# Kernel tuning notes

Hardware: AMD Instinct MI355X
Metric: run time of the kernel (lower is better)

The kernel has to match this reference:

```python
import jax, jax.numpy as jnp
import numpy as np

H_HEADS = 16
STATE_N = 64

def setup_inputs() -> dict:
    key = jax.random.key(0)
    ks = jax.random.split(key, 9)
    B, T, D = 2, 1024, 1024
    H, ch, N = H_HEADS, D // H_HEADS, STATE_N
    inp = jax.random.normal(ks[0], (B, T, D), dtype=jnp.float32)
    # lin_logA params scaled so exp(cumsum(logA)) stays bounded (decaying state)
    W_logA = jax.random.normal(ks[1], (H, 1, ch), dtype=jnp.float32) * 0.01
    b_logA = jnp.full((H, 1), -0.05, dtype=jnp.float32)
    W_XBC = jax.random.normal(ks[3], (H, ch + 2 * N, ch), dtype=jnp.float32) * (1.0 / np.sqrt(ch))
    b_XBC = jax.random.normal(ks[4], (H, ch + 2 * N), dtype=jnp.float32) * 0.02
    W_gate = jax.random.normal(ks[5], (H, ch, ch), dtype=jnp.float32) * (1.0 / np.sqrt(ch))
    b_gate = jax.random.normal(ks[6], (H, ch), dtype=jnp.float32) * 0.02
    W_out = jax.random.normal(ks[7], (D, D), dtype=jnp.float32) * (1.0 / np.sqrt(D))
    b_out = jax.random.normal(ks[8], (D,), dtype=jnp.float32) * 0.02
    return {"inp": inp, "W_logA": W_logA, "b_logA": b_logA, "W_XBC": W_XBC,
            "b_XBC": b_XBC, "W_gate": W_gate, "b_gate": b_gate,
            "W_out": W_out, "b_out": b_out}

def _mamba2_forward(inp, W_logA, b_logA, W_XBC, b_XBC, W_gate, b_gate, W_out, b_out):
    B, T, D = inp.shape
    H, N = H_HEADS, STATE_N
    ch = D // H
    x = inp.reshape(B, T, H, ch)  # B,T,H,ch
    # MultiheadLinear: matmul((H,out,in), x[...,None]) + bias
    logA = jnp.einsum('hoc,bthc->btho', W_logA, x)[..., 0] + b_logA[:, 0]  # B,T,H
    XBC = jax.nn.silu(jnp.einsum('hoc,bthc->btho', W_XBC, x) + b_XBC)     # B,T,H,ch+2N
    X = XBC[..., :ch]                 # B,T,H,ch
    Bm = XBC[..., ch:ch + N]          # B,T,H,N
    Cm = XBC[..., ch + N:]            # B,T,H,N
    # quadratic SSM: A_ss[b,h,i,j] = exp(cum[i]-cum[j]) for j<=i else 0
    cum = jnp.cumsum(jnp.swapaxes(logA, 1, 2), axis=-1)  # B,H,T
    diff = cum[..., :, None] - cum[..., None, :]          # B,H,T,T
    causal = jnp.tril(jnp.ones((T, T), dtype=bool))
    A_ss = jnp.where(causal, jnp.exp(jnp.where(causal, diff, 0.0)), 0.0)  # B,H,T,T
    G = jnp.einsum('bihn,bjhn->bhij', Cm, Bm)             # B,H,T,T (C_i . B_j)
    Y = jnp.einsum('bhij,bjhc->bihc', A_ss * G, X)        # B,T,H,ch
    gate = jnp.einsum('hoc,bthc->btho', W_gate, x) + b_gate
    Yg = (gate * Y).reshape(B, T, D)
    return Yg @ W_out.T + b_out

def reference(inp, W_logA, b_logA, W_XBC, b_XBC, W_gate, b_gate, W_out, b_out):
    return _mamba2_forward(inp, W_logA, b_logA, W_XBC, b_XBC, W_gate, b_gate, W_out, b_out)
```

## Files before the change

kernel.cpp:

```cpp
#include <hip/hip_runtime.h>

typedef unsigned int   u32;
typedef unsigned short u16;
typedef __attribute__((ext_vector_type(8))) short bf16x8;
typedef __attribute__((ext_vector_type(4))) float f32x4;

__device__ __forceinline__ float bfs(u16 u) {
  union { u32 i; float f; } v; v.i = ((u32)u) << 16; return v.f;
}
__device__ __forceinline__ u16 f2bf(float f) {
  union { float f; u32 i; } v; v.f = f;
  u32 r = v.i + 0x7fffu + ((v.i >> 16) & 1u);
  return (u16)(r >> 16);
}
__device__ __forceinline__ ushort4 f2bf4(float4 v) {
  ushort4 p; p.x = f2bf(v.x); p.y = f2bf(v.y); p.z = f2bf(v.z); p.w = f2bf(v.w);
  return p;
}

__global__ __launch_bounds__(256) void k_proj(
    const float* __restrict__ inp,
    const float* __restrict__ W_XBC,  const float* __restrict__ b_XBC,
    const float* __restrict__ W_gate, const float* __restrict__ b_gate,
    const float* __restrict__ W_logA, const float* __restrict__ b_logA,
    u16* __restrict__ XsT, u16* __restrict__ Bms, u16* __restrict__ Cms,
    u16* __restrict__ gates, float* __restrict__ logAs)
{
  int tt = blockIdx.x, h = blockIdx.y;
  int tid = threadIdx.x;
  int w = tid >> 6, l = tid & 63, q = l >> 4, lr = l & 15;
  int m0 = tt * 64;
  int b = m0 >> 10, tl0 = m0 & 1023;
  int bh = b * 16 + h;

  __shared__ u16 Xt[64][72];
  __shared__ u16 Wt[256][72];
  __shared__ float wl[64];

  if (tid < 64) wl[tid] = W_logA[h * 64 + tid];
#pragma unroll
  for (int i = 0; i < 4; ++i) {
    int f = tid + 256 * i; int r = f >> 4, cq = f & 15;
    float4 xv = *(const float4*)(inp + (size_t)(m0 + r) * 1024 + h * 64 + 4 * cq);
    *(ushort4*)&Xt[r][4 * cq] = f2bf4(xv);
  }
#pragma unroll
  for (int i = 0; i < 16; ++i) {
    int f = tid + 256 * i; int r = f >> 4, cq = f & 15;
    const float* wsrc = (r < 192) ? (W_XBC + ((size_t)h * 192 + r) * 64)
                                  : (W_gate + ((size_t)h * 64 + (r - 192)) * 64);
    *(ushort4*)&Wt[r][4 * cq] = f2bf4(*(const float4*)(wsrc + 4 * cq));
  }
  __syncthreads();

  bf16x8 af[4][2];
#pragma unroll
  for (int rt = 0; rt < 4; ++rt) {
    af[rt][0] = *(const bf16x8*)&Xt[16 * rt + lr][q * 8];
    af[rt][1] = *(const bf16x8*)&Xt[16 * rt + lr][32 + q * 8];
  }

  f32x4 acc[4][4];
#pragma unroll
  for (int rt = 0; rt < 4; ++rt)
#pragma unroll
    for (int ct = 0; ct < 4; ++ct) acc[rt][ct] = (f32x4){0.f, 0.f, 0.f, 0.f};

#pragma unroll
  for (int ct = 0; ct < 4; ++ct) {
    bf16x8 b0 = *(const bf16x8*)&Wt[64 * w + 16 * ct + lr][q * 8];
    bf16x8 b1 = *(const bf16x8*)&Wt[64 * w + 16 * ct + lr][32 + q * 8];
#pragma unroll
    for (int rt = 0; rt < 4; ++rt) {
      acc[rt][ct] = __builtin_amdgcn_mfma_f32_16x16x32_bf16(af[rt][0], b0, acc[rt][ct], 0, 0, 0);
      acc[rt][ct] = __builtin_amdgcn_mfma_f32_16x16x32_bf16(af[rt][1], b1, acc[rt][ct], 0, 0, 0);
    }
  }

  if (tid < 64) {
    float a = b_logA[h];
#pragma unroll 16
    for (int k = 0; k < 64; ++k) a += bfs(Xt[tid][k]) * wl[k];
    logAs[(size_t)bh * 1024 + tl0 + tid] = a;
  }

  if (w == 0) {
#pragma unroll
    for (int ct = 0; ct < 4; ++ct) {
      int n = 16 * ct + lr;
      float bias = b_XBC[h * 192 + n];
#pragma unroll
      for (int rt = 0; rt < 4; ++rt) {
        float4 v;
#pragma unroll
        for (int r = 0; r < 4; ++r) {
          float s = acc[rt][ct][r] + bias;
          (&v.x)[r] = s / (1.f + __expf(-s));
        }
        *(ushort4*)(XsT + ((size_t)bh * 64 + n) * 1024 + tl0 + 16 * rt + q * 4) = f2bf4(v);
      }
    }
  } else if (w < 3) {
    u16* dst = (w == 1) ? Bms : Cms;
    int nbase = h * 192 + 64 * w;
#pragma unroll
    for (int ct = 0; ct < 4; ++ct) {
      int n = 16 * ct + lr;
      float bias = b_XBC[nbase + n];
#pragma unroll
      for (int rt = 0; rt < 4; ++rt)
#pragma unroll
        for (int r = 0; r < 4; ++r) {
          int tloc = tl0 + 16 * rt + q * 4 + r;
          float s = acc[rt][ct][r] + bias;
          s = s / (1.f + __expf(-s));
          dst[((size_t)bh * 1024 + tloc) * 64 + n] = f2bf(s);
        }
    }
  } else {
#pragma unroll
    for (int ct = 0; ct < 4; ++ct) {
      int n = 16 * ct + lr;
      float bias = b_gate[h * 64 + n];
#pragma unroll
      for (int rt = 0; rt < 4; ++rt)
#pragma unroll
        for (int r = 0; r < 4; ++r) {
          int tg = m0 + 16 * rt + q * 4 + r;
          gates[((size_t)tg * 16 + h) * 64 + n] = f2bf(acc[rt][ct][r] + bias);
        }
    }
  }
}

__global__ __launch_bounds__(1024) void k_scan(float* __restrict__ logAs)
{
  int bh = blockIdx.x;
  int t = threadIdx.x;
  __shared__ float buf0[1024], buf1[1024];
  buf0[t] = logAs[(size_t)bh * 1024 + t];
  __syncthreads();
  float* src = buf0; float* dstp = buf1;
  for (int off = 1; off < 1024; off <<= 1) {
    float v = src[t];
    if (t >= off) v += src[t - off];
    dstp[t] = v;
    __syncthreads();
    float* tmp = src; src = dstp; dstp = tmp;
  }
  logAs[(size_t)bh * 1024 + t] = src[t];
}

__global__ __launch_bounds__(256) void k_wconv(
    const float* __restrict__ Wout, u16* __restrict__ WoutB)
{
  int i = blockIdx.x * 256 + threadIdx.x;
  float4 v = ((const float4*)Wout)[i];
  ((ushort4*)WoutB)[i] = f2bf4(v);
}

__global__ __launch_bounds__(256) void k_ssm(
    const u16* __restrict__ XsT, const u16* __restrict__ Bms, const u16* __restrict__ Cms,
    const float* __restrict__ cum, const u16* __restrict__ gates, u16* __restrict__ Yg)
{
  int g = blockIdx.x >> 5;
  int bh = blockIdx.x & 31;
  int it = (g & 1) ? (g >> 1) : (15 - (g >> 1));
  int b = bh >> 4, h = bh & 15;

  const u16* Xb = XsT + (size_t)bh * 64 * 1024;
  const u16* Bb = Bms + (size_t)bh * 1024 * 64;
  const u16* Cb = Cms + (size_t)bh * 1024 * 64;
  const float* cumb = cum + bh * 1024;

  int tid = threadIdx.x;
  int w = tid >> 6, l = tid & 63, q = l >> 4, lr = l & 15;

  __shared__ u16 Cts[64][72];
  __shared__ u16 Bts[64][72];
  __shared__ u16 Xts[64][72];
  __shared__ u16 Sts[64][72];
  __shared__ float cumi[64], cumj[64];

  int i0 = it * 64;
#pragma unroll
  for (int i = 0; i < 4; ++i) {
    int f = tid + 256 * i; int r = f >> 4, cq = f & 15;
    *(ushort4*)&Cts[r][4 * cq] = *(const ushort4*)(Cb + (size_t)(i0 + r) * 64 + 4 * cq);
  }
  if (tid < 64) cumi[tid] = cumb[i0 + tid];
  __syncthreads();

  bf16x8 ca0 = *(const bf16x8*)&Cts[16 * w + lr][q * 8];
  bf16x8 ca1 = *(const bf16x8*)&Cts[16 * w + lr][32 + q * 8];

  f32x4 acc[4];
#pragma unroll
  for (int ct = 0; ct < 4; ++ct) acc[ct] = (f32x4){0.f, 0.f, 0.f, 0.f};

  for (int jt = 0; jt <= it; ++jt) {
    int j0 = jt * 64;
    __syncthreads();
#pragma unroll
    for (int i = 0; i < 4; ++i) {
      int f = tid + 256 * i; int r = f >> 4, cq = f & 15;
      *(ushort4*)&Bts[r][4 * cq] = *(const ushort4*)(Bb + (size_t)(j0 + r) * 64 + 4 * cq);
      *(ushort4*)&Xts[r][4 * cq] = *(const ushort4*)(Xb + (size_t)r * 1024 + j0 + 4 * cq);
    }
    if (tid < 64) cumj[tid] = cumb[j0 + tid];
    __syncthreads();

    bool diag = (jt == it);
#pragma unroll
    for (int ct = 0; ct < 4; ++ct) {
      f32x4 s = (f32x4){0.f, 0.f, 0.f, 0.f};
      bf16x8 b0 = *(const bf16x8*)&Bts[16 * ct + lr][q * 8];
      bf16x8 b1 = *(const bf16x8*)&Bts[16 * ct + lr][32 + q * 8];
      s = __builtin_amdgcn_mfma_f32_16x16x32_bf16(ca0, b0, s, 0, 0, 0);
      s = __builtin_amdgcn_mfma_f32_16x16x32_bf16(ca1, b1, s, 0, 0, 0);
      int jl = 16 * ct + lr;
      float cj = cumj[jl];
#pragma unroll
      for (int r = 0; r < 4; ++r) {
        int il = 16 * w + q * 4 + r;
        float v;
        if (diag && jl > il) v = 0.f;
        else v = s[r] * __expf(fminf(cumi[il] - cj, 30.f));
        Sts[il][jl] = f2bf(v);
      }
    }

    bf16x8 sa0 = *(const bf16x8*)&Sts[16 * w + lr][q * 8];
    bf16x8 sa1 = *(const bf16x8*)&Sts[16 * w + lr][32 + q * 8];
#pragma unroll
    for (int ct = 0; ct < 4; ++ct) {
      bf16x8 x0 = *(const bf16x8*)&Xts[16 * ct + lr][q * 8];
      bf16x8 x1 = *(const bf16x8*)&Xts[16 * ct + lr][32 + q * 8];
      acc[ct] = __builtin_amdgcn_mfma_f32_16x16x32_bf16(sa0, x0, acc[ct], 0, 0, 0);
      acc[ct] = __builtin_amdgcn_mfma_f32_16x16x32_bf16(sa1, x1, acc[ct], 0, 0, 0);
    }
  }

#pragma unroll
  for (int ct = 0; ct < 4; ++ct) {
    int c = 16 * ct + lr;
#pragma unroll
    for (int r = 0; r < 4; ++r) {
      int tg = i0 + 16 * w + q * 4 + r;
      size_t row = (size_t)(b * 1024 + tg);
      float gt = bfs(gates[(row * 16 + h) * 64 + c]);
      Yg[row * 1024 + h * 64 + c] = f2bf(acc[ct][r] * gt);
    }
  }
}

__global__ __launch_bounds__(256) void k_out(
    const u16* __restrict__ Yg, const u16* __restrict__ WoutB,
    const float* __restrict__ bout, float* __restrict__ out)
{
  int bm = blockIdx.x, bn = blockIdx.y;
  int tid = threadIdx.x;
  int w = tid >> 6, l = tid & 63, q = l >> 4, lr = l & 15;
  int m0 = bm * 128, d0 = bn * 64;

  __shared__ u16 Yt[128][72];
  __shared__ u16 Wt[64][72];

  f32x4 acc[2][4];
#pragma unroll
  for (int rt = 0; rt < 2; ++rt)
#pragma unroll
    for (int ct = 0; ct < 4; ++ct) acc[rt][ct] = (f32x4){0.f, 0.f, 0.f, 0.f};

  for (int kt = 0; kt < 16; ++kt) {
    int k0 = kt * 64;
#pragma unroll
    for (int i = 0; i < 8; ++i) {
      int f = tid + 256 * i; int r = f >> 4, cq = f & 15;
      *(ushort4*)&Yt[r][4 * cq] = *(const ushort4*)(Yg + (size_t)(m0 + r) * 1024 + k0 + 4 * cq);
    }
#pragma unroll
    for (int i = 0; i < 4; ++i) {
      int f = tid + 256 * i; int r = f >> 4, cq = f & 15;
      *(ushort4*)&Wt[r][4 * cq] = *(const ushort4*)(WoutB + (size_t)(d0 + r) * 1024 + k0 + 4 * cq);
    }
    __syncthreads();

    bf16x8 a00 = *(const bf16x8*)&Yt[32 * w + lr][q * 8];
    bf16x8 a01 = *(const bf16x8*)&Yt[32 * w + lr][32 + q * 8];
    bf16x8 a10 = *(const bf16x8*)&Yt[32 * w + 16 + lr][q * 8];
    bf16x8 a11 = *(const bf16x8*)&Yt[32 * w + 16 + lr][32 + q * 8];
#pragma unroll
    for (int ct = 0; ct < 4; ++ct) {
      bf16x8 b0 = *(const bf16x8*)&Wt[16 * ct + lr][q * 8];
      bf16x8 b1 = *(const bf16x8*)&Wt[16 * ct + lr][32 + q * 8];
      acc[0][ct] = __builtin_amdgcn_mfma_f32_16x16x32_bf16(a00, b0, acc[0][ct], 0, 0, 0);
      acc[0][ct] = __builtin_amdgcn_mfma_f32_16x16x32_bf16(a01, b1, acc[0][ct], 0, 0, 0);
      acc[1][ct] = __builtin_amdgcn_mfma_f32_16x16x32_bf16(a10, b0, acc[1][ct], 0, 0, 0);
      acc[1][ct] = __builtin_amdgcn_mfma_f32_16x16x32_bf16(a11, b1, acc[1][ct], 0, 0, 0);
    }
    __syncthreads();
  }

#pragma unroll
  for (int rt = 0; rt < 2; ++rt)
#pragma unroll
    for (int ct = 0; ct < 4; ++ct) {
      int d = d0 + 16 * ct + lr;
      float bo = bout[d];
#pragma unroll
      for (int r = 0; r < 4; ++r) {
        int m = m0 + 32 * w + 16 * rt + q * 4 + r;
        out[(size_t)m * 1024 + d] = acc[rt][ct][r] + bo;
      }
    }
}

extern "C" void kernel_launch(void* const* d_in, const int* in_sizes, int n_in,
                              void* d_out, int out_size, void* d_ws, size_t ws_size,
                              hipStream_t stream)
{
  const float* inp   = (const float*)d_in[0];
  const float* WlogA = (const float*)d_in[1];
  const float* blogA = (const float*)d_in[2];
  const float* WXBC  = (const float*)d_in[3];
  const float* bXBC  = (const float*)d_in[4];
  const float* Wgate = (const float*)d_in[5];
  const float* bgate = (const float*)d_in[6];
  const float* Wout  = (const float*)d_in[7];
  const float* bout  = (const float*)d_in[8];
  float* out = (float*)d_out;

  const size_t SZ = (size_t)2 * 16 * 1024 * 64;
  float* logAs = (float*)d_ws;
  u16* base16  = (u16*)(logAs + 32768);
  u16* XsT   = base16;
  u16* Bms   = XsT + SZ;
  u16* Cms   = Bms + SZ;
  u16* gates = Cms + SZ;
  u16* Yg    = gates + SZ;
  u16* WoutB = Yg + SZ;

  k_proj<<<dim3(32, 16), 256, 0, stream>>>(inp, WXBC, bXBC, Wgate, bgate,
                                           WlogA, blogA, XsT, Bms, Cms, gates, logAs);
  k_scan<<<32, 1024, 0, stream>>>(logAs);
  k_wconv<<<1024, 256, 0, stream>>>(Wout, WoutB);
  k_ssm<<<dim3(512), 256, 0, stream>>>(XsT, Bms, Cms, logAs, gates, Yg);
  k_out<<<dim3(16, 16), 256, 0, stream>>>(Yg, WoutB, bout, out);
}
```

Before: 137.4 us.

## Factor decay exp, prefetch tiles in SSM and output GEMM, shuffle-based scan

The scan kernel becomes a warp-shuffle prefix sum and also writes exp(cum) and exp(-cum) per timestep. The SSM kernel then multiplies these factors instead of computing an exponential per score element. Both the SSM and output-projection kernels now prefetch the next K/B/X tiles into registers while computing the current one. The output GEMM uses 512 threads per block, with each wave handling 16 rows. The factorised exponent drops the old clamp, so large cumulative decay could overflow or lose precision.

```diff
diff --git a/kernel.cpp b/kernel.cpp
--- a/kernel.cpp
+++ b/kernel.cpp
@@ -133,22 +133,35 @@
   }
 }
 
-__global__ __launch_bounds__(1024) void k_scan(float* __restrict__ logAs)
+__global__ __launch_bounds__(1024) void k_scan(
+    const float* __restrict__ logAs, float* __restrict__ rowexp,
+    float* __restrict__ colexp)
 {
   int bh = blockIdx.x;
   int t = threadIdx.x;
-  __shared__ float buf0[1024], buf1[1024];
-  buf0[t] = logAs[(size_t)bh * 1024 + t];
+  int wv = t >> 6, ln = t & 63;
+  __shared__ float wsum[16];
+  float v = logAs[(size_t)bh * 1024 + t];
+#pragma unroll
+  for (int off = 1; off < 64; off <<= 1) {
+    float n = __shfl_up(v, off, 64);
+    if (ln >= off) v += n;
+  }
+  if (ln == 63) wsum[wv] = v;
   __syncthreads();
-  float* src = buf0; float* dstp = buf1;
-  for (int off = 1; off < 1024; off <<= 1) {
-    float v = src[t];
-    if (t >= off) v += src[t - off];
-    dstp[t] = v;
-    __syncthreads();
-    float* tmp = src; src = dstp; dstp = tmp;
-  }
-  logAs[(size_t)bh * 1024 + t] = src[t];
+  if (wv == 0) {
+    float s = (ln < 16) ? wsum[ln] : 0.f;
+#pragma unroll
+    for (int off = 1; off < 16; off <<= 1) {
+      float n = __shfl_up(s, off, 64);
+      if (ln >= off) s += n;
+    }
+    if (ln < 16) wsum[ln] = s;
+  }
+  __syncthreads();
+  if (wv > 0) v += wsum[wv - 1];
+  rowexp[(size_t)bh * 1024 + t] = __expf(v);
+  colexp[(size_t)bh * 1024 + t] = __expf(-v);
 }
 
 __global__ __launch_bounds__(256) void k_wconv(
@@ -161,7 +174,8 @@
 
 __global__ __launch_bounds__(256) void k_ssm(
     const u16* __restrict__ XsT, const u16* __restrict__ Bms, const u16* __restrict__ Cms,
-    const float* __restrict__ cum, const u16* __restrict__ gates, u16* __restrict__ Yg)
+    const float* __restrict__ rowexp, const float* __restrict__ colexp,
+    const u16* __restrict__ gates, u16* __restrict__ Yg)
 {
   int g = blockIdx.x >> 5;
   int bh = blockIdx.x & 31;
@@ -171,7 +185,6 @@
   const u16* Xb = XsT + (size_t)bh * 64 * 1024;
   const u16* Bb = Bms + (size_t)bh * 1024 * 64;
   const u16* Cb = Cms + (size_t)bh * 1024 * 64;
-  const float* cumb = cum + bh * 1024;
 
   int tid = threadIdx.x;
   int w = tid >> 6, l = tid & 63, q = l >> 4, lr = l & 15;
@@ -180,7 +193,7 @@
   __shared__ u16 Bts[64][72];
   __shared__ u16 Xts[64][72];
   __shared__ u16 Sts[64][72];
-  __shared__ float cumi[64], cumj[64];
+  __shared__ float ref_[64], cef[64];
 
   int i0 = it * 64;
 #pragma unroll
@@ -188,7 +201,7 @@
     int f = tid + 256 * i; int r = f >> 4, cq = f & 15;
     *(ushort4*)&Cts[r][4 * cq] = *(const ushort4*)(Cb + (size_t)(i0 + r) * 64 + 4 * cq);
   }
-  if (tid < 64) cumi[tid] = cumb[i0 + tid];
+  if (tid < 64) ref_[tid] = rowexp[(size_t)bh * 1024 + i0 + tid];
   __syncthreads();
 
   bf16x8 ca0 = *(const bf16x8*)&Cts[16 * w + lr][q * 8];
@@ -198,17 +211,36 @@
 #pragma unroll
   for (int ct = 0; ct < 4; ++ct) acc[ct] = (f32x4){0.f, 0.f, 0.f, 0.f};
 
+  ushort4 pb[4], px[4]; float pce = 0.f;
+#pragma unroll
+  for (int i = 0; i < 4; ++i) {
+    int f = tid + 256 * i; int r = f >> 4, cq = f & 15;
+    pb[i] = *(const ushort4*)(Bb + (size_t)r * 64 + 4 * cq);
+    px[i] = *(const ushort4*)(Xb + (size_t)r * 1024 + 4 * cq);
+  }
+  if (tid < 64) pce = colexp[(size_t)bh * 1024 + tid];
+
   for (int jt = 0; jt <= it; ++jt) {
-    int j0 = jt * 64;
     __syncthreads();
 #pragma unroll
     for (int i = 0; i < 4; ++i) {
       int f = tid + 256 * i; int r = f >> 4, cq = f & 15;
-      *(ushort4*)&Bts[r][4 * cq] = *(const ushort4*)(Bb + (size_t)(j0 + r) * 64 + 4 * cq);
-      *(ushort4*)&Xts[r][4 * cq] = *(const ushort4*)(Xb + (size_t)r * 1024 + j0 + 4 * cq);
-    }
-    if (tid < 64) cumj[tid] = cumb[j0 + tid];
+      *(ushort4*)&Bts[r][4 * cq] = pb[i];
+      *(ushort4*)&Xts[r][4 * cq] = px[i];
+    }
+    if (tid < 64) cef[tid] = pce;
     __syncthreads();
+
+    if (jt < it) {
+      int j1 = (jt + 1) * 64;
+#pragma unroll
+      for (int i = 0; i < 4; ++i) {
+        int f = tid + 256 * i; int r = f >> 4, cq = f & 15;
+        pb[i] = *(const ushort4*)(Bb + (size_t)(j1 + r) * 64 + 4 * cq);
+        px[i] = *(const ushort4*)(Xb + (size_t)r * 1024 + j1 + 4 * cq);
+      }
+      if (tid < 64) pce = colexp[(size_t)bh * 1024 + j1 + tid];
+    }
 
     bool diag = (jt == it);
 #pragma unroll
@@ -219,13 +251,11 @@
       s = __builtin_amdgcn_mfma_f32_16x16x32_bf16(ca0, b0, s, 0, 0, 0);
       s = __builtin_amdgcn_mfma_f32_16x16x32_bf16(ca1, b1, s, 0, 0, 0);
       int jl = 16 * ct + lr;
-      float cj = cumj[jl];
+      float cj = cef[jl];
 #pragma unroll
       for (int r = 0; r < 4; ++r) {
         int il = 16 * w + q * 4 + r;
-        float v;
-        if (diag && jl > il) v = 0.f;
-        else v = s[r] * __expf(fminf(cumi[il] - cj, 30.f));
+        float v = (diag && jl > il) ? 0.f : s[r] * ref_[il] * cj;
         Sts[il][jl] = f2bf(v);
       }
     }
@@ -254,7 +284,7 @@
   }
 }
 
-__global__ __launch_bounds__(256) void k_out(
+__global__ __launch_bounds__(512) void k_out(
     const u16* __restrict__ Yg, const u16* __restrict__ WoutB,
     const float* __restrict__ bout, float* __restrict__ out)
 {
@@ -266,54 +296,71 @@
   __shared__ u16 Yt[128][72];
   __shared__ u16 Wt[64][72];
 
-  f32x4 acc[2][4];
-#pragma unroll
-  for (int rt = 0; rt < 2; ++rt)
-#pragma unroll
-    for (int ct = 0; ct < 4; ++ct) acc[rt][ct] = (f32x4){0.f, 0.f, 0.f, 0.f};
+  f32x4 acc[4];
+#pragma unroll
+  for (int ct = 0; ct < 4; ++ct) acc[ct] = (f32x4){0.f, 0.f, 0.f, 0.f};
+
+  ushort4 py[4], pw[2];
+#pragma unroll
+  for (int i = 0; i < 4; ++i) {
+    int f = tid + 512 * i; int r = f >> 4, cq = f & 15;
+    py[i] = *(const ushort4*)(Yg + (size_t)(m0 + r) * 1024 + 4 * cq);
+  }
+#pragma unroll
+  for (int i = 0; i < 2; ++i) {
+    int f = tid + 512 * i; int r = f >> 4, cq = f & 15;
+    pw[i] = *(const ushort4*)(WoutB + (size_t)(d0 + r) * 1024 + 4 * cq);
+  }
 
   for (int kt = 0; kt < 16; ++kt) {
-    int k0 = kt * 64;
-#pragma unroll
-    for (int i = 0; i < 8; ++i) {
-      int f = tid + 256 * i; int r = f >> 4, cq = f & 15;
-      *(ushort4*)&Yt[r][4 * cq] = *(const ushort4*)(Yg + (size_t)(m0 + r) * 1024 + k0 + 4 * cq);
-    }
+    __syncthreads();
 #pragma unroll
     for (int i = 0; i < 4; ++i) {
-      int f = tid + 256 * i; int r = f >> 4, cq = f & 15;
-      *(ushort4*)&Wt[r][4 * cq] = *(const ushort4*)(WoutB + (size_t)(d0 + r) * 1024 + k0 + 4 * cq);
+      int f = tid + 512 * i; int r = f >> 4, cq = f & 15;
+      *(ushort4*)&Yt[r][4 * cq] = py[i];
+    }
+#pragma unroll
+    for (int i = 0; i < 2; ++i) {
+      int f = tid + 512 * i; int r = f >> 4, cq = f & 15;
+      *(ushort4*)&Wt[r][4 * cq] = pw[i];
     }
     __syncthreads();
 
-    bf16x8 a00 = *(const bf16x8*)&Yt[32 * w + lr][q * 8];
-    bf16x8 a01 = *(const bf16x8*)&Yt[32 * w + lr][32 + q * 8];
-    bf16x8 a10 = *(const bf16x8*)&Yt[32 * w + 16 + lr][q * 8];
-    bf16x8 a11 = *(const bf16x8*)&Yt[32 * w + 16 + lr][32 + q * 8];
+    if (kt < 15) {
+      int k1 = (kt + 1) * 64;
+#pragma unroll
+      for (int i = 0; i < 4; ++i) {
+        int f = tid + 512 * i; int r = f >> 4, cq = f & 15;
+        py[i] = *(const ushort4*)(Yg + (size_t)(m0 + r) * 1024 + k1 + 4 * cq);
+      }
+#pragma unroll
+      for (int i = 0; i < 2; ++i) {
+        int f = tid + 512 * i; int r = f >> 4, cq = f & 15;
+        pw[i] = *(const ushort4*)(WoutB + (size_t)(d0 + r) * 1024 + k1 + 4 * cq);
+      }
+    }
+
+    bf16x8 a0 = *(const bf16x8*)&Yt[16 * w + lr][q * 8];
+    bf16x8 a1 = *(const bf16x8*)&Yt[16 * w + lr][32 + q * 8];
 #pragma unroll
     for (int ct = 0; ct < 4; ++ct) {
       bf16x8 b0 = *(const bf16x8*)&Wt[16 * ct + lr][q * 8];
       bf16x8 b1 = *(const bf16x8*)&Wt[16 * ct + lr][32 + q * 8];
-      acc[0][ct] = __builtin_amdgcn_mfma_f32_16x16x32_bf16(a00, b0, acc[0][ct], 0, 0, 0);
-      acc[0][ct] = __builtin_amdgcn_mfma_f32_16x16x32_bf16(a01, b1, acc[0][ct], 0, 0, 0);
-      acc[1][ct] = __builtin_amdgcn_mfma_f32_16x16x32_bf16(a10, b0, acc[1][ct], 0, 0, 0);
-      acc[1][ct] = __builtin_amdgcn_mfma_f32_16x16x32_bf16(a11, b1, acc[1][ct], 0, 0, 0);
-    }
-    __syncthreads();
-  }
-
-#pragma unroll
-  for (int rt = 0; rt < 2; ++rt)
-#pragma unroll
-    for (int ct = 0; ct < 4; ++ct) {
-      int d = d0 + 16 * ct + lr;
-      float bo = bout[d];
-#pragma unroll
-      for (int r = 0; r < 4; ++r) {
-        int m = m0 + 32 * w + 16 * rt + q * 4 + r;
-        out[(size_t)m * 1024 + d] = acc[rt][ct][r] + bo;
-      }
-    }
+      acc[ct] = __builtin_amdgcn_mfma_f32_16x16x32_bf16(a0, b0, acc[ct], 0, 0, 0);
+      acc[ct] = __builtin_amdgcn_mfma_f32_16x16x32_bf16(a1, b1, acc[ct], 0, 0, 0);
+    }
+  }
+
+#pragma unroll
+  for (int ct = 0; ct < 4; ++ct) {
+    int d = d0 + 16 * ct + lr;
+    float bo = bout[d];
+#pragma unroll
+    for (int r = 0; r < 4; ++r) {
+      int m = m0 + 16 * w + q * 4 + r;
+      out[(size_t)m * 1024 + d] = acc[ct][r] + bo;
+    }
+  }
 }
 
 extern "C" void kernel_launch(void* const* d_in, const int* in_sizes, int n_in,
@@ -332,8 +379,10 @@
   float* out = (float*)d_out;
 
   const size_t SZ = (size_t)2 * 16 * 1024 * 64;
-  float* logAs = (float*)d_ws;
-  u16* base16  = (u16*)(logAs + 32768);
+  float* logAs  = (float*)d_ws;
+  float* rowexp = logAs + 32768;
+  float* colexp = rowexp + 32768;
+  u16* base16  = (u16*)(colexp + 32768);
   u16* XsT   = base16;
   u16* Bms   = XsT + SZ;
   u16* Cms   = Bms + SZ;
@@ -343,8 +392,8 @@
 
   k_proj<<<dim3(32, 16), 256, 0, stream>>>(inp, WXBC, bXBC, Wgate, bgate,
                                            WlogA, blogA, XsT, Bms, Cms, gates, logAs);
-  k_scan<<<32, 1024, 0, stream>>>(logAs);
+  k_scan<<<32, 1024, 0, stream>>>(logAs, rowexp, colexp);
   k_wconv<<<1024, 256, 0, stream>>>(Wout, WoutB);
-  k_ssm<<<dim3(512), 256, 0, stream>>>(XsT, Bms, Cms, logAs, gates, Yg);
-  k_out<<<dim3(16, 16), 256, 0, stream>>>(Yg, WoutB, bout, out);
-}
+  k_ssm<<<dim3(512), 256, 0, stream>>>(XsT, Bms, Cms, rowexp, colexp, gates, Yg);
+  k_out<<<dim3(16, 16), 512, 0, stream>>>(Yg, WoutB, bout, out);
+}
```

Result: faster. 128.9 us (-6.2%).
